# Kernel tuning notes

Hardware: AMD Instinct MI355X
Metric: run time of the kernel (lower is better)

The kernel has to match this reference:

```python
import jax, jax.numpy as jnp
import numpy as np


def setup_inputs() -> dict:
    key = jax.random.key(0)
    ks = jax.random.split(key, 8)
    B, H, W, C = 4, 64, 64, 256
    d = C // 8  # 32
    s = 0.02
    return {
        "x": jax.random.normal(ks[0], (B, H, W, C), dtype=jnp.float32),
        "Wq": jax.random.normal(ks[1], (C, d), dtype=jnp.float32) * s,
        "bq": jnp.zeros((d,), dtype=jnp.float32),
        "Wk": jax.random.normal(ks[2], (C, d), dtype=jnp.float32) * s,
        "bk": jnp.zeros((d,), dtype=jnp.float32),
        "Wv": jax.random.normal(ks[3], (C, C), dtype=jnp.float32) * s,
        "bv": jnp.zeros((C,), dtype=jnp.float32),
        "gamma": jnp.zeros((1,), dtype=jnp.float32),
    }


def reference(x, Wq, bq, Wk, bk, Wv, bv, gamma):
    B, H, W, C = x.shape
    N = H * W
    xf = x.reshape(B, N, C)                       # 1x1 conv == per-pixel matmul
    q = xf @ Wq + bq                              # [B, N, C//8]
    k = xf @ Wk + bk                              # [B, N, C//8]
    v = xf @ Wv + bv                              # [B, N, C]
    attn = jax.nn.softmax(jnp.einsum('bnd,bmd->bnm', q, k), axis=-1)  # [B, N, N]
    out = jnp.einsum('bnm,bmc->bnc', attn, v).reshape(B, H, W, C)
    return gamma * out + x
```

## Files before the change

### kernel.cpp

```cpp
#include <hip/hip_runtime.h>
#include <hip/hip_bf16.h>

typedef __bf16 bf16;
typedef __bf16 bf16x8 __attribute__((ext_vector_type(8)));
typedef float f32x4 __attribute__((ext_vector_type(4)));

static __device__ __forceinline__ f32x4 mfma16(bf16x8 a, bf16x8 b, f32x4 c) {
  return __builtin_amdgcn_mfma_f32_16x16x32_bf16(a, b, c, 0, 0, 0);
}

static __device__ __forceinline__ bf16x8 cvt8(const float* p) {
  f32x4 a0 = *(const f32x4*)p;
  f32x4 a1 = *(const f32x4*)(p + 4);
  bf16x8 r;
#pragma unroll
  for (int j = 0; j < 4; ++j) { r[j] = (bf16)a0[j]; r[4 + j] = (bf16)a1[j]; }
  return r;
}

__global__ void prep_wt(const float* __restrict__ Wq, const float* __restrict__ Wk,
                        const float* __restrict__ Wv, bf16* __restrict__ Wt) {
  int k = blockIdx.x;
  int c = threadIdx.x;
  float v;
  if (c < 32)       v = Wq[k * 32 + c];
  else if (c < 64)  v = Wk[k * 32 + (c - 32)];
  else              v = Wv[k * 256 + (c - 64)];
  Wt[c * 256 + k] = (bf16)v;
}

__global__ __launch_bounds__(256) void qkv_gemm(
    const float* __restrict__ x, const bf16* __restrict__ Wt,
    const float* __restrict__ bq, const float* __restrict__ bk,
    const float* __restrict__ bv,
    bf16* __restrict__ Qd, bf16* __restrict__ Kd, bf16* __restrict__ Vt) {
  __shared__ __align__(16) bf16 tile[64 * 72];
  int tid = threadIdx.x;
  int lane = tid & 63, w = tid >> 6;
  int lw = lane & 15, qq = lane >> 4;
  int r0 = blockIdx.x * 64;
  int bb = r0 >> 12, n0 = r0 & 4095;

  const float* arow = x + (size_t)(r0 + 16 * w + lw) * 256;
  bf16x8 a[8];
#pragma unroll
  for (int kc = 0; kc < 8; ++kc) a[kc] = cvt8(arow + kc * 32 + qq * 8);

  for (int c0 = 0; c0 < 320; c0 += 64) {
    f32x4 acc[4] = {};
#pragma unroll
    for (int kc = 0; kc < 8; ++kc)
#pragma unroll
      for (int t = 0; t < 4; ++t) {
        bf16x8 b = *(const bf16x8*)(Wt + (size_t)(c0 + 16 * t + lw) * 256 + kc * 32 + qq * 8);
        acc[t] = mfma16(a[kc], b, acc[t]);
      }
    if (c0 == 0) {
#pragma unroll
      for (int t = 0; t < 4; ++t) {
        int c = 16 * t + lw;
        float bias = (c < 32) ? bq[c] : bk[c - 32];
#pragma unroll
        for (int i = 0; i < 4; ++i) {
          int n = n0 + 16 * w + 4 * qq + i;
          bf16 hv = (bf16)(acc[t][i] + bias);
          if (c < 32) Qd[((size_t)(bb << 12) + n) * 32 + c] = hv;
          else        Kd[((size_t)(bb << 12) + n) * 32 + (c - 32)] = hv;
        }
      }
    } else {
#pragma unroll
      for (int t = 0; t < 4; ++t) {
        int cl = 16 * t + lw;
        float bias = bv[c0 - 64 + cl];
#pragma unroll
        for (int i = 0; i < 4; ++i)
          tile[cl * 72 + 16 * w + 4 * qq + i] = (bf16)(acc[t][i] + bias);
      }
      __syncthreads();
      int nl = tid & 63;
#pragma unroll
      for (int it = 0; it < 16; ++it) {
        int cl = 4 * it + w;
        Vt[((size_t)bb * 256 + (c0 - 64) + cl) * 4096 + n0 + nl] = tile[cl * 72 + nl];
      }
      __syncthreads();
    }
  }
}

__global__ __launch_bounds__(512, 2) void flash_attn(
    const bf16* __restrict__ Qd, const bf16* __restrict__ Kd,
    const bf16* __restrict__ Vt, const float* __restrict__ x,
    const float* __restrict__ gamma, float* __restrict__ out) {
  __shared__ __align__(16) bf16 Pl[2][64 * 72];
  __shared__ __align__(16) float lsum2[2][64];

  int tid = threadIdx.x;
  int lane = tid & 63, w = tid >> 6;
  int lw = lane & 15, qq = lane >> 4;
  int wr = w & 3, wc = w >> 2, chb = 32 * w;
  int bb = blockIdx.y;
  int r0 = blockIdx.x * 64;

  const bf16* Qb = Qd + ((size_t)bb << 12) * 32;
  const bf16* Kb = Kd + ((size_t)bb << 12) * 32;
  const bf16* Vb = Vt + (size_t)bb * 256 * 4096;

  bf16x8 qf = *(const bf16x8*)(Qb + (size_t)(r0 + 16 * wr + lw) * 32 + qq * 8);

  f32x4 o[4][2] = {};
  float l_part[4] = {};
  bf16x8 kbuf0[2], kbuf1[2], vbuf0[4], vbuf1[4];

#pragma unroll
  for (int t = 0; t < 2; ++t)
    kbuf0[t] = *(const bf16x8*)(Kb + (size_t)(32 * wc + 16 * t + lw) * 32 + qq * 8);
  {
    f32x4 s[2];
#pragma unroll
    for (int t = 0; t < 2; ++t) { f32x4 z = {}; s[t] = mfma16(qf, kbuf0[t], z); }
#pragma unroll
    for (int t = 0; t < 2; ++t)
#pragma unroll
      for (int i = 0; i < 4; ++i) {
        float p = __expf(s[t][i]);
        l_part[i] += p;
        Pl[0][(16 * wr + 4 * qq + i) * 72 + 32 * wc + 16 * t + lw] = (bf16)p;
      }
  }
#pragma unroll
  for (int t = 0; t < 2; ++t)
    kbuf1[t] = *(const bf16x8*)(Kb + (size_t)(64 + 32 * wc + 16 * t + lw) * 32 + qq * 8);
#pragma unroll
  for (int t = 0; t < 2; ++t)
#pragma unroll
    for (int kc = 0; kc < 2; ++kc)
      vbuf0[t * 2 + kc] = *(const bf16x8*)(Vb + (size_t)(chb + 16 * t + lw) * 4096 + kc * 32 + qq * 8);
  __syncthreads();

#define FA_BODY(J, PCUR, PNXT, KN, KC, VC, VN)                                     \
  {                                                                                \
    const int j = (J);                                                             \
    int n1 = ((j + 1) & 63) * 64, n2 = ((j + 2) & 63) * 64;                        \
    bf16x8 af[4][2];                                                               \
    _Pragma("unroll") for (int m = 0; m < 4; ++m)                                  \
      _Pragma("unroll") for (int kc = 0; kc < 2; ++kc)                             \
        af[m][kc] = *(const bf16x8*)&Pl[PCUR][(16 * m + lw) * 72 + kc * 32 + qq * 8]; \
    if (j < 63) {                                                                  \
      f32x4 s[2];                                                                  \
      _Pragma("unroll") for (int t = 0; t < 2; ++t) {                              \
        f32x4 z = {};                                                              \
        s[t] = mfma16(qf, KN[t], z);                                               \
      }                                                                            \
      _Pragma("unroll") for (int t = 0; t < 2; ++t)                                \
        _Pragma("unroll") for (int i = 0; i < 4; ++i) {                            \
          float p = __expf(s[t][i]);                                               \
          l_part[i] += p;                                                          \
          Pl[PNXT][(16 * wr + 4 * qq + i) * 72 + 32 * wc + 16 * t + lw] = (bf16)p; \
        }                                                                          \
      _Pragma("unroll") for (int t = 0; t < 2; ++t)                                \
        KC[t] = *(const bf16x8*)(Kb + (size_t)(n2 + 32 * wc + 16 * t + lw) * 32 + qq * 8); \
    }                                                                              \
    _Pragma("unroll") for (int t = 0; t < 2; ++t)                                  \
      _Pragma("unroll") for (int kc = 0; kc < 2; ++kc)                             \
        VN[t * 2 + kc] = *(const bf16x8*)(Vb + (size_t)(chb + 16 * t + lw) * 4096 + n1 + kc * 32 + qq * 8); \
    _Pragma("unroll") for (int kc = 0; kc < 2; ++kc)                               \
      _Pragma("unroll") for (int t = 0; t < 2; ++t)                                \
        _Pragma("unroll") for (int m = 0; m < 4; ++m)                              \
          o[m][t] = mfma16(af[m][kc], VC[t * 2 + kc], o[m][t]);                    \
    __syncthreads();                                                               \
  }

  for (int jj = 0; jj < 32; ++jj) {
    FA_BODY(2 * jj,     0, 1, kbuf1, kbuf0, vbuf0, vbuf1)
    FA_BODY(2 * jj + 1, 1, 0, kbuf0, kbuf1, vbuf1, vbuf0)
  }
#undef FA_BODY

#pragma unroll
  for (int i = 0; i < 4; ++i) {
    float v = l_part[i];
    v += __shfl_xor(v, 1);
    v += __shfl_xor(v, 2);
    v += __shfl_xor(v, 4);
    v += __shfl_xor(v, 8);
    if (lw == 0) lsum2[wc][16 * wr + 4 * qq + i] = v;
  }
  __syncthreads();

  float g = gamma[0];
#pragma unroll
  for (int m = 0; m < 4; ++m) {
    f32x4 la = *(const f32x4*)&lsum2[0][16 * m + 4 * qq];
    f32x4 lb = *(const f32x4*)&lsum2[1][16 * m + 4 * qq];
#pragma unroll
    for (int i = 0; i < 4; ++i) {
      float rinv = 1.f / (la[i] + lb[i]);
      int row = r0 + 16 * m + 4 * qq + i;
      size_t base = (((size_t)bb << 12) + row) * 256 + chb;
#pragma unroll
      for (int t = 0; t < 2; ++t)
        out[base + 16 * t + lw] = g * (o[m][t][i] * rinv) + x[base + 16 * t + lw];
    }
  }
}

extern "C" void kernel_launch(void* const* d_in, const int* in_sizes, int n_in,
                              void* d_out, int out_size, void* d_ws, size_t ws_size,
                              hipStream_t stream) {
  const float* x     = (const float*)d_in[0];
  const float* Wq    = (const float*)d_in[1];
  const float* bq    = (const float*)d_in[2];
  const float* Wk    = (const float*)d_in[3];
  const float* bk    = (const float*)d_in[4];
  const float* Wv    = (const float*)d_in[5];
  const float* bv    = (const float*)d_in[6];
  const float* gamma = (const float*)d_in[7];
  float* out = (float*)d_out;

  const size_t WT_E = 320 * 256;
  const size_t QK_E = (size_t)4096 * 32;
  const size_t VT_E = (size_t)256 * 4096;
  size_t full_bytes = (WT_E + 4 * 2 * QK_E + 4 * VT_E) * sizeof(bf16);

  bf16* Wt = (bf16*)d_ws;
  prep_wt<<<dim3(256), dim3(320), 0, stream>>>(Wq, Wk, Wv, Wt);

  if (ws_size >= full_bytes) {
    bf16* Qd = Wt + WT_E;
    bf16* Kd = Qd + 4 * QK_E;
    bf16* Vt = Kd + 4 * QK_E;
    qkv_gemm<<<dim3(256), dim3(256), 0, stream>>>(x, Wt, bq, bk, bv, Qd, Kd, Vt);
    flash_attn<<<dim3(64, 4), dim3(512), 0, stream>>>(Qd, Kd, Vt, x, gamma, out);
  } else {
    bf16* Qd = Wt + WT_E;
    bf16* Kd = Qd + QK_E;
    bf16* Vt = Kd + QK_E;
    for (int b = 0; b < 4; ++b) {
      const float* xb = x + (size_t)b * 4096 * 256;
      float* outb = out + (size_t)b * 4096 * 256;
      qkv_gemm<<<dim3(64), dim3(256), 0, stream>>>(xb, Wt, bq, bk, bv, Qd, Kd, Vt);
      flash_attn<<<dim3(64, 1), dim3(512), 0, stream>>>(Qd, Kd, Vt, xb, gamma, outb);
    }
  }
}
```

Baseline: 182.4 us.

## Split attention channels across grid z and parallelize QKV GEMM column tiles

Flash attention now launches two blocks per query tile, each producing 128 output channels, doubling grid size while duplicating the QK^T and softmax exponent computation. The QKV projection distributes its five 64-column tiles across grid y instead of looping in one block, reloading x per tile. The weight transpose kernel swaps block/thread roles for coalesced reads. The aim is better CU occupancy on a wide GPU at the cost of redundant score computation and extra x reads.

```diff
diff --git a/kernel.cpp b/kernel.cpp
--- a/kernel.cpp
+++ b/kernel.cpp
@@ -20,8 +20,8 @@
 
 __global__ void prep_wt(const float* __restrict__ Wq, const float* __restrict__ Wk,
                         const float* __restrict__ Wv, bf16* __restrict__ Wt) {
-  int k = blockIdx.x;
-  int c = threadIdx.x;
+  int c = blockIdx.x;
+  int k = threadIdx.x;
   float v;
   if (c < 32)       v = Wq[k * 32 + c];
   else if (c < 64)  v = Wk[k * 32 + (c - 32)];
@@ -38,53 +38,48 @@
   int tid = threadIdx.x;
   int lane = tid & 63, w = tid >> 6;
   int lw = lane & 15, qq = lane >> 4;
-  int r0 = blockIdx.x * 64;
+  int r0 = blockIdx.x * 64, c0 = blockIdx.y * 64;
   int bb = r0 >> 12, n0 = r0 & 4095;
 
   const float* arow = x + (size_t)(r0 + 16 * w + lw) * 256;
-  bf16x8 a[8];
-#pragma unroll
-  for (int kc = 0; kc < 8; ++kc) a[kc] = cvt8(arow + kc * 32 + qq * 8);
-
-  for (int c0 = 0; c0 < 320; c0 += 64) {
-    f32x4 acc[4] = {};
-#pragma unroll
-    for (int kc = 0; kc < 8; ++kc)
-#pragma unroll
-      for (int t = 0; t < 4; ++t) {
-        bf16x8 b = *(const bf16x8*)(Wt + (size_t)(c0 + 16 * t + lw) * 256 + kc * 32 + qq * 8);
-        acc[t] = mfma16(a[kc], b, acc[t]);
+  f32x4 acc[4] = {};
+#pragma unroll
+  for (int kc = 0; kc < 8; ++kc) {
+    bf16x8 a = cvt8(arow + kc * 32 + qq * 8);
+#pragma unroll
+    for (int t = 0; t < 4; ++t) {
+      bf16x8 b = *(const bf16x8*)(Wt + (size_t)(c0 + 16 * t + lw) * 256 + kc * 32 + qq * 8);
+      acc[t] = mfma16(a, b, acc[t]);
+    }
+  }
+  if (c0 == 0) {
+#pragma unroll
+    for (int t = 0; t < 4; ++t) {
+      int c = 16 * t + lw;
+      float bias = (c < 32) ? bq[c] : bk[c - 32];
+#pragma unroll
+      for (int i = 0; i < 4; ++i) {
+        int n = n0 + 16 * w + 4 * qq + i;
+        bf16 hv = (bf16)(acc[t][i] + bias);
+        if (c < 32) Qd[((size_t)(bb << 12) + n) * 32 + c] = hv;
+        else        Kd[((size_t)(bb << 12) + n) * 32 + (c - 32)] = hv;
       }
-    if (c0 == 0) {
-#pragma unroll
-      for (int t = 0; t < 4; ++t) {
-        int c = 16 * t + lw;
-        float bias = (c < 32) ? bq[c] : bk[c - 32];
-#pragma unroll
-        for (int i = 0; i < 4; ++i) {
-          int n = n0 + 16 * w + 4 * qq + i;
-          bf16 hv = (bf16)(acc[t][i] + bias);
-          if (c < 32) Qd[((size_t)(bb << 12) + n) * 32 + c] = hv;
-          else        Kd[((size_t)(bb << 12) + n) * 32 + (c - 32)] = hv;
-        }
-      }
-    } else {
-#pragma unroll
-      for (int t = 0; t < 4; ++t) {
-        int cl = 16 * t + lw;
-        float bias = bv[c0 - 64 + cl];
-#pragma unroll
-        for (int i = 0; i < 4; ++i)
-          tile[cl * 72 + 16 * w + 4 * qq + i] = (bf16)(acc[t][i] + bias);
-      }
-      __syncthreads();
-      int nl = tid & 63;
-#pragma unroll
-      for (int it = 0; it < 16; ++it) {
-        int cl = 4 * it + w;
-        Vt[((size_t)bb * 256 + (c0 - 64) + cl) * 4096 + n0 + nl] = tile[cl * 72 + nl];
-      }
-      __syncthreads();
+    }
+  } else {
+#pragma unroll
+    for (int t = 0; t < 4; ++t) {
+      int cl = 16 * t + lw;
+      float bias = bv[c0 - 64 + cl];
+#pragma unroll
+      for (int i = 0; i < 4; ++i)
+        tile[cl * 72 + 16 * w + 4 * qq + i] = (bf16)(acc[t][i] + bias);
+    }
+    __syncthreads();
+    int nl = tid & 63;
+#pragma unroll
+    for (int it = 0; it < 16; ++it) {
+      int cl = 4 * it + w;
+      Vt[((size_t)bb * 256 + (c0 - 64) + cl) * 4096 + n0 + nl] = tile[cl * 72 + nl];
     }
   }
 }
@@ -99,9 +94,10 @@
   int tid = threadIdx.x;
   int lane = tid & 63, w = tid >> 6;
   int lw = lane & 15, qq = lane >> 4;
-  int wr = w & 3, wc = w >> 2, chb = 32 * w;
+  int wr = w & 3, wc = w >> 2;
   int bb = blockIdx.y;
   int r0 = blockIdx.x * 64;
+  int chb = blockIdx.z * 128 + 16 * w;
 
   const bf16* Qb = Qd + ((size_t)bb << 12) * 32;
   const bf16* Kb = Kd + ((size_t)bb << 12) * 32;
@@ -109,9 +105,9 @@
 
   bf16x8 qf = *(const bf16x8*)(Qb + (size_t)(r0 + 16 * wr + lw) * 32 + qq * 8);
 
-  f32x4 o[4][2] = {};
+  f32x4 o[4] = {};
   float l_part[4] = {};
-  bf16x8 kbuf0[2], kbuf1[2], vbuf0[4], vbuf1[4];
+  bf16x8 kbuf0[2], kbuf1[2], vbuf0[2], vbuf1[2];
 
 #pragma unroll
   for (int t = 0; t < 2; ++t)
@@ -133,10 +129,8 @@
   for (int t = 0; t < 2; ++t)
     kbuf1[t] = *(const bf16x8*)(Kb + (size_t)(64 + 32 * wc + 16 * t + lw) * 32 + qq * 8);
 #pragma unroll
-  for (int t = 0; t < 2; ++t)
-#pragma unroll
-    for (int kc = 0; kc < 2; ++kc)
-      vbuf0[t * 2 + kc] = *(const bf16x8*)(Vb + (size_t)(chb + 16 * t + lw) * 4096 + kc * 32 + qq * 8);
+  for (int kc = 0; kc < 2; ++kc)
+    vbuf0[kc] = *(const bf16x8*)(Vb + (size_t)(chb + lw) * 4096 + kc * 32 + qq * 8);
   __syncthreads();
 
 #define FA_BODY(J, PCUR, PNXT, KN, KC, VC, VN)                                     \
@@ -162,13 +156,11 @@
       _Pragma("unroll") for (int t = 0; t < 2; ++t)                                \
         KC[t] = *(const bf16x8*)(Kb + (size_t)(n2 + 32 * wc + 16 * t + lw) * 32 + qq * 8); \
     }                                                                              \
-    _Pragma("unroll") for (int t = 0; t < 2; ++t)                                  \
-      _Pragma("unroll") for (int kc = 0; kc < 2; ++kc)                             \
-        VN[t * 2 + kc] = *(const bf16x8*)(Vb + (size_t)(chb + 16 * t + lw) * 4096 + n1 + kc * 32 + qq * 8); \
     _Pragma("unroll") for (int kc = 0; kc < 2; ++kc)                               \
-      _Pragma("unroll") for (int t = 0; t < 2; ++t)                                \
-        _Pragma("unroll") for (int m = 0; m < 4; ++m)                              \
-          o[m][t] = mfma16(af[m][kc], VC[t * 2 + kc], o[m][t]);                    \
+      VN[kc] = *(const bf16x8*)(Vb + (size_t)(chb + lw) * 4096 + n1 + kc * 32 + qq * 8); \
+    _Pragma("unroll") for (int kc = 0; kc < 2; ++kc)                               \
+      _Pragma("unroll") for (int m = 0; m < 4; ++m)                                \
+        o[m] = mfma16(af[m][kc], VC[kc], o[m]);                                    \
     __syncthreads();                                                               \
   }
 
@@ -199,9 +191,7 @@
       float rinv = 1.f / (la[i] + lb[i]);
       int row = r0 + 16 * m + 4 * qq + i;
       size_t base = (((size_t)bb << 12) + row) * 256 + chb;
-#pragma unroll
-      for (int t = 0; t < 2; ++t)
-        out[base + 16 * t + lw] = g * (o[m][t][i] * rinv) + x[base + 16 * t + lw];
+      out[base + lw] = g * (o[m][i] * rinv) + x[base + lw];
     }
   }
 }
@@ -225,14 +215,14 @@
   size_t full_bytes = (WT_E + 4 * 2 * QK_E + 4 * VT_E) * sizeof(bf16);
 
   bf16* Wt = (bf16*)d_ws;
-  prep_wt<<<dim3(256), dim3(320), 0, stream>>>(Wq, Wk, Wv, Wt);
+  prep_wt<<<dim3(320), dim3(256), 0, stream>>>(Wq, Wk, Wv, Wt);
 
   if (ws_size >= full_bytes) {
     bf16* Qd = Wt + WT_E;
     bf16* Kd = Qd + 4 * QK_E;
     bf16* Vt = Kd + 4 * QK_E;
-    qkv_gemm<<<dim3(256), dim3(256), 0, stream>>>(x, Wt, bq, bk, bv, Qd, Kd, Vt);
-    flash_attn<<<dim3(64, 4), dim3(512), 0, stream>>>(Qd, Kd, Vt, x, gamma, out);
+    qkv_gemm<<<dim3(256, 5), dim3(256), 0, stream>>>(x, Wt, bq, bk, bv, Qd, Kd, Vt);
+    flash_attn<<<dim3(64, 4, 2), dim3(512), 0, stream>>>(Qd, Kd, Vt, x, gamma, out);
   } else {
     bf16* Qd = Wt + WT_E;
     bf16* Kd = Qd + QK_E;
@@ -240,8 +230,8 @@
     for (int b = 0; b < 4; ++b) {
       const float* xb = x + (size_t)b * 4096 * 256;
       float* outb = out + (size_t)b * 4096 * 256;
-      qkv_gemm<<<dim3(64), dim3(256), 0, stream>>>(xb, Wt, bq, bk, bv, Qd, Kd, Vt);
-      flash_attn<<<dim3(64, 1), dim3(512), 0, stream>>>(Qd, Kd, Vt, xb, gamma, outb);
-    }
-  }
-}
+      qkv_gemm<<<dim3(64, 5), dim3(256), 0, stream>>>(xb, Wt, bq, bk, bv, Qd, Kd, Vt);
+      flash_attn<<<dim3(64, 1, 2), dim3(512), 0, stream>>>(Qd, Kd, Vt, xb, gamma, outb);
+    }
+  }
+}
```

Result: slower. 199.4 us (+9.4%).
